# Kernel tuning notes

Hardware: AMD Instinct MI355X
Metric: run time of the kernel (lower is better)

## Reference

```python
import jax, jax.numpy as jnp
import numpy as np

B, S, D, H = 1, 4096, 1024, 16
HD = D // H  # head_dim = 64


def setup_inputs() -> dict:
    key = jax.random.key(0)
    k1, k2, k3 = jax.random.split(key, 3)
    scale = 0.02
    return {
        "x": jax.random.normal(k1, (B, S, D), dtype=jnp.float32),
        "w_qkv": jax.random.normal(k2, (D, 3 * D), dtype=jnp.float32) * scale,
        "b_qkv": jnp.zeros((3 * D,), dtype=jnp.float32),
        "w_proj": jax.random.normal(k3, (D, D), dtype=jnp.float32) * scale,
        "b_proj": jnp.zeros((D,), dtype=jnp.float32),
    }


def reference(x, w_qkv, b_qkv, w_proj, b_proj):
    b, s, d = x.shape
    qkv = x @ w_qkv + b_qkv                      # [b, s, 3d]
    q, k, v = jnp.split(qkv, 3, axis=-1)
    # [b, h, s, hd]
    q = q.reshape(b, s, H, HD).transpose(0, 2, 1, 3)
    k = k.reshape(b, s, H, HD).transpose(0, 2, 1, 3)
    v = v.reshape(b, s, H, HD).transpose(0, 2, 1, 3)
    score = jnp.einsum("bhqd,bhkd->bhqk", q, k) / jnp.sqrt(jnp.float32(HD))
    causal = jnp.tril(jnp.ones((s, s), dtype=bool))
    score = jnp.where(causal, score, -jnp.inf)
    attn = jax.nn.softmax(score, axis=-1)        # dropout omitted (eval mode, p effectively 0)
    out = jnp.einsum("bhqk,bhkd->bhqd", attn, v)  # [b, h, s, hd]
    out = out.transpose(0, 2, 1, 3).reshape(b, s, d)
    return out @ w_proj + b_proj
```

## Files before the change

kernel.cpp:

```cpp
#include <hip/hip_runtime.h>
#include <hip/hip_bf16.h>
#include <math.h>

typedef __bf16 bf16;
typedef __bf16 bf16x8 __attribute__((ext_vector_type(8)));
typedef __bf16 bf16x4 __attribute__((ext_vector_type(4)));
typedef float f32x4 __attribute__((ext_vector_type(4)));

#define S_ 4096
#define D_ 1024
#define H_ 16
#define HD_ 64
#define N3_ 3072

typedef const __attribute__((address_space(1))) void* gas1_t;
typedef __attribute__((address_space(3))) void* las3_t;
static __device__ __forceinline__ void g2l16(const void* g, void* l) {
  __builtin_amdgcn_global_load_lds((gas1_t)g, (las3_t)l, 16, 0, 0);
}

__global__ __launch_bounds__(256) void cvt_f32_bf16(const float* __restrict__ in,
                                                    bf16* __restrict__ out) {
  int i = (blockIdx.x * 256 + threadIdx.x) * 4;
  float4 v = *(const float4*)(in + i);
  bf16x4 o;
  o.x = (bf16)v.x; o.y = (bf16)v.y; o.z = (bf16)v.z; o.w = (bf16)v.w;
  *(bf16x4*)(out + i) = o;
}

__global__ __launch_bounds__(256) void transpose_f32_bf16(const float* __restrict__ in,
                                                          bf16* __restrict__ out,
                                                          int R, int C, int ldin, int col0) {
  __shared__ float t[32][33];
  int bx = blockIdx.x * 32;
  int by = blockIdx.y * 32;
  int tx = threadIdx.x & 31, ty = threadIdx.x >> 5;
#pragma unroll
  for (int i = 0; i < 4; ++i)
    t[ty + i * 8][tx] = in[(size_t)(by + ty + i * 8) * ldin + col0 + bx + tx];
  __syncthreads();
#pragma unroll
  for (int i = 0; i < 4; ++i)
    out[(size_t)(bx + ty + i * 8) * R + by + tx] = (bf16)t[tx][ty + i * 8];
}

__global__ __launch_bounds__(256) void transpose_bf16(const bf16* __restrict__ in,
                                                      bf16* __restrict__ out,
                                                      int R, int C, int ldin, int col0) {
  __shared__ bf16 t[32][33];
  int bx = blockIdx.x * 32;
  int by = blockIdx.y * 32;
  int tx = threadIdx.x & 31, ty = threadIdx.x >> 5;
#pragma unroll
  for (int i = 0; i < 4; ++i)
    t[ty + i * 8][tx] = in[(size_t)(by + ty + i * 8) * ldin + col0 + bx + tx];
  __syncthreads();
#pragma unroll
  for (int i = 0; i < 4; ++i)
    out[(size_t)(bx + ty + i * 8) * R + by + tx] = t[tx][ty + i * 8];
}

template <int BN>
__global__ __launch_bounds__(256) void gemm_bt(const bf16* __restrict__ A,
                                               const bf16* __restrict__ Bt,
                                               const float* __restrict__ bias,
                                               bf16* __restrict__ outb,
                                               float* __restrict__ outf,
                                               int M, int N, int K,
                                               int qlim, float qscale) {
  constexpr int NT = BN / 32;
  __shared__ bf16 sA[128 * 32];
  __shared__ bf16 sB[BN * 32];
  const int tid = threadIdx.x;
  const int wave = tid >> 6, lane = tid & 63;
  const int col = lane & 15, quad = lane >> 4;
  const int wm = (wave & 1) * 64, wn = (wave >> 1) * (BN / 2);
  const long bm = (long)blockIdx.x * 128, bn = (long)blockIdx.y * BN;
  const int srow = tid >> 2;
  const int soff = (tid & 3) * 8;

  f32x4 acc[4][NT] = {};

  for (int kb = 0; kb < K; kb += 32) {
    __syncthreads();
    g2l16(A + (bm + srow) * (long)K + kb + soff,      &sA[tid * 8]);
    g2l16(A + (bm + 64 + srow) * (long)K + kb + soff, &sA[2048 + tid * 8]);
#pragma unroll
    for (int i = 0; i < BN / 64; ++i)
      g2l16(Bt + (bn + i * 64 + srow) * (long)K + kb + soff, &sB[i * 2048 + tid * 8]);
    __syncthreads();

    bf16x8 af[4], bfr[NT];
#pragma unroll
    for (int t = 0; t < 4; ++t)
      af[t] = *(const bf16x8*)(&sA[(wm + t * 16 + col) * 32 + quad * 8]);
#pragma unroll
    for (int t = 0; t < NT; ++t)
      bfr[t] = *(const bf16x8*)(&sB[(wn + t * 16 + col) * 32 + quad * 8]);
#pragma unroll
    for (int mt = 0; mt < 4; ++mt)
#pragma unroll
      for (int nt = 0; nt < NT; ++nt)
        acc[mt][nt] = __builtin_amdgcn_mfma_f32_16x16x32_bf16(af[mt], bfr[nt], acc[mt][nt], 0, 0, 0);
  }

#pragma unroll
  for (int mt = 0; mt < 4; ++mt) {
#pragma unroll
    for (int nt = 0; nt < NT; ++nt) {
      long gn = bn + wn + nt * 16 + col;
      float bv = bias ? bias[gn] : 0.f;
      float sc = (gn < qlim) ? qscale : 1.0f;
#pragma unroll
      for (int i = 0; i < 4; ++i) {
        long gm = bm + wm + mt * 16 + quad * 4 + i;
        float v = (acc[mt][nt][i] + bv) * sc;
        if (outf) outf[gm * N + gn] = v;
        else      outb[gm * N + gn] = (bf16)v;
      }
    }
  }
}

__device__ __forceinline__ int swz_g(int row) {
  return (row & 3) | ((((row >> 2) ^ (row >> 3)) & 1) << 2);
}

__global__ __launch_bounds__(256) void attn_kernel(const bf16* __restrict__ qkv,
                                                   const bf16* __restrict__ vT,
                                                   bf16* __restrict__ Opart,
                                                   float* __restrict__ lws) {
  __shared__ bf16 sK[2][64 * 64];
  __shared__ bf16 sV[2][64 * 64];
  const int hh = blockIdx.x;
  const int qb = (int)(gridDim.y - 1 - blockIdx.y);
  const int sp = blockIdx.z;
  const int tid = threadIdx.x;
  const int wave = tid >> 6, lane = tid & 63;
  const int col = lane & 15, quad = lane >> 4;
  const int qbase = qb * 128 + wave * 32;

  const bf16* qp0 = qkv + (size_t)(qbase + col) * N3_ + hh * HD_;
  bf16x8 aq[2][2];
  aq[0][0] = *(const bf16x8*)(qp0 + quad * 8);
  aq[0][1] = *(const bf16x8*)(qp0 + 32 + quad * 8);
  aq[1][0] = *(const bf16x8*)(qp0 + 16 * N3_ + quad * 8);
  aq[1][1] = *(const bf16x8*)(qp0 + 16 * N3_ + 32 + quad * 8);

  bf16x8 ones;
#pragma unroll
  for (int j = 0; j < 8; ++j) ones[j] = (bf16)1.0f;

  f32x4 acc[2][4] = {};
  f32x4 acc_l[2] = {};

  const bf16* kgbase = qkv + D_ + hh * HD_;
  const bf16* vgbase = vT + (size_t)hh * HD_ * S_;
  const int krow = (col >> 2) * 8 + (col & 3);
  const int it0 = sp ? (qb + 1) : 0;
  const int it1 = sp ? 2 * (qb + 1) : (qb + 1);

  const int srow = tid >> 2;
  const int sc0 = (tid & 3) * 2;
  const int gs = swz_g(srow);
  const int soff0 = srow * 64 + ((sc0 ^ gs) * 8);
  const int soff1 = srow * 64 + (((sc0 + 1) ^ gs) * 8);

  {
    const bf16* kg = kgbase + (size_t)(it0 * 64 + srow) * N3_ + sc0 * 8;
    const bf16* vg = vgbase + (size_t)srow * S_ + it0 * 64 + sc0 * 8;
    *(int4*)(&sK[0][soff0]) = *(const int4*)kg;
    *(int4*)(&sK[0][soff1]) = *(const int4*)(kg + 8);
    *(int4*)(&sV[0][soff0]) = *(const int4*)vg;
    *(int4*)(&sV[0][soff1]) = *(const int4*)(vg + 8);
  }
  __syncthreads();

  for (int j = it0; j < it1; ++j) {
    const int kb = j * 64;
    const int cur = (j - it0) & 1;
    const bool more = (j + 1 < it1);
    int4 pk0, pk1, pv0, pv1;
    if (more) {
      const bf16* kg = kgbase + (size_t)(kb + 64 + srow) * N3_ + sc0 * 8;
      const bf16* vg = vgbase + (size_t)srow * S_ + kb + 64 + sc0 * 8;
      pk0 = *(const int4*)kg; pk1 = *(const int4*)(kg + 8);
      pv0 = *(const int4*)vg; pv1 = *(const int4*)(vg + 8);
    }

    if (kb < qbase + 32) {
      const bool act0 = kb < qbase + 16;
      const bf16* kc = &sK[cur][0];
      const bf16* vc = &sV[cur][0];

      f32x4 st[2][4];
#pragma unroll
      for (int t = 0; t < 4; ++t) {
        int row = (t >> 1) * 32 + (t & 1) * 4 + krow;
        int pc = quad ^ swz_g(row);
        bf16x8 bk0 = *(const bf16x8*)(kc + row * 64 + pc * 8);
        bf16x8 bk1 = *(const bf16x8*)(kc + row * 64 + (pc ^ 4) * 8);
        if (act0) {
          f32x4 z = {};
          z = __builtin_amdgcn_mfma_f32_16x16x32_bf16(bk0, aq[0][0], z, 0, 0, 0);
          st[0][t] = __builtin_amdgcn_mfma_f32_16x16x32_bf16(bk1, aq[0][1], z, 0, 0, 0);
        }
        f32x4 z = {};
        z = __builtin_amdgcn_mfma_f32_16x16x32_bf16(bk0, aq[1][0], z, 0, 0, 0);
        st[1][t] = __builtin_amdgcn_mfma_f32_16x16x32_bf16(bk1, aq[1][1], z, 0, 0, 0);
      }

      bf16x8 pfrag[2][2];
#pragma unroll
      for (int s2 = 0; s2 < 2; ++s2) {
        if (s2 == 0 && !act0) continue;
        const int rowbase = qbase + 16 * s2;
        float p[4][4];
        if (kb + 63 <= rowbase) {
#pragma unroll
          for (int t = 0; t < 4; ++t)
#pragma unroll
            for (int r = 0; r < 4; ++r)
              p[t][r] = __builtin_amdgcn_exp2f(st[s2][t][r]);
        } else {
#pragma unroll
          for (int t = 0; t < 4; ++t)
#pragma unroll
            for (int r = 0; r < 4; ++r) {
              int key = kb + (t >> 1) * 32 + quad * 8 + (t & 1) * 4 + r;
              p[t][r] = (key > rowbase + col)
                            ? 0.f
                            : __builtin_amdgcn_exp2f(st[s2][t][r]);
            }
        }
#pragma unroll
        for (int c = 0; c < 2; ++c)
#pragma unroll
          for (int j2 = 0; j2 < 4; ++j2) {
            pfrag[s2][c][j2]     = (bf16)p[2 * c][j2];
            pfrag[s2][c][j2 + 4] = (bf16)p[2 * c + 1][j2];
          }
      }

#pragma unroll
      for (int c = 0; c < 2; ++c) {
#pragma unroll
        for (int n = 0; n < 4; ++n) {
          int row = n * 16 + col;
          int pc = (4 * c + quad) ^ swz_g(row);
          bf16x8 bv = *(const bf16x8*)(vc + row * 64 + pc * 8);
          if (act0)
            acc[0][n] = __builtin_amdgcn_mfma_f32_16x16x32_bf16(pfrag[0][c], bv, acc[0][n], 0, 0, 0);
          acc[1][n] = __builtin_amdgcn_mfma_f32_16x16x32_bf16(pfrag[1][c], bv, acc[1][n], 0, 0, 0);
        }
        if (act0)
          acc_l[0] = __builtin_amdgcn_mfma_f32_16x16x32_bf16(pfrag[0][c], ones, acc_l[0], 0, 0, 0);
        acc_l[1] = __builtin_amdgcn_mfma_f32_16x16x32_bf16(pfrag[1][c], ones, acc_l[1], 0, 0, 0);
      }
    }

    if (more) {
      bf16* kn = &sK[cur ^ 1][0];
      bf16* vn = &sV[cur ^ 1][0];
      *(int4*)(kn + soff0) = pk0;
      *(int4*)(kn + soff1) = pk1;
      *(int4*)(vn + soff0) = pv0;
      *(int4*)(vn + soff1) = pv1;
    }
    __syncthreads();
  }

  bf16* Op = Opart + (size_t)sp * S_ * D_;
#pragma unroll
  for (int s2 = 0; s2 < 2; ++s2) {
    const int rowbase = qbase + 16 * s2;
    if (col == 0) {
#pragma unroll
      for (int r = 0; r < 4; ++r)
        lws[((size_t)sp * H_ + hh) * S_ + rowbase + quad * 4 + r] = acc_l[s2][r];
    }
#pragma unroll
    for (int n = 0; n < 4; ++n)
#pragma unroll
      for (int r = 0; r < 4; ++r)
        Op[(size_t)(rowbase + quad * 4 + r) * D_ + hh * HD_ + n * 16 + col] =
            (bf16)acc[s2][n][r];
  }
}

__global__ __launch_bounds__(256) void attn_combine(const bf16* __restrict__ Opart,
                                                    const float* __restrict__ lws,
                                                    bf16* __restrict__ outb) {
  int e = (blockIdx.x * 256 + threadIdx.x) * 8;
  int s = e >> 10;
  int d = e & (D_ - 1);
  int h = d >> 6;
  float l = lws[(size_t)h * S_ + s] + lws[((size_t)H_ + h) * S_ + s];
  float inv = 1.0f / l;
  bf16x8 a = *(const bf16x8*)(Opart + e);
  bf16x8 b = *(const bf16x8*)(Opart + (size_t)S_ * D_ + e);
  bf16x8 o;
#pragma unroll
  for (int j = 0; j < 8; ++j)
    o[j] = (bf16)(((float)a[j] + (float)b[j]) * inv);
  *(bf16x8*)(outb + e) = o;
}

extern "C" void kernel_launch(void* const* d_in, const int* in_sizes, int n_in,
                              void* d_out, int out_size, void* d_ws, size_t ws_size,
                              hipStream_t stream) {
  const float* x      = (const float*)d_in[0];
  const float* w_qkv  = (const float*)d_in[1];
  const float* b_qkv  = (const float*)d_in[2];
  const float* w_proj = (const float*)d_in[3];
  const float* b_proj = (const float*)d_in[4];
  float* out = (float*)d_out;

  bf16* xb     = (bf16*)d_ws;
  bf16* wqkvT  = xb + (size_t)S_ * D_;
  bf16* wprojT = wqkvT + (size_t)N3_ * D_;
  bf16* qkv    = wprojT + (size_t)D_ * D_;
  bf16* vT     = qkv + (size_t)S_ * N3_;
  bf16* attn   = vT + (size_t)D_ * S_;
  bf16* Opart  = attn + (size_t)S_ * D_;
  float* lws   = (float*)(Opart + (size_t)2 * S_ * D_);

  const float QSCALE = 0.125f * 1.44269504088896f;

  cvt_f32_bf16<<<dim3((S_ * D_) / 1024), 256, 0, stream>>>(x, xb);
  transpose_f32_bf16<<<dim3(N3_ / 32, D_ / 32), 256, 0, stream>>>(w_qkv, wqkvT, D_, N3_, N3_, 0);
  transpose_f32_bf16<<<dim3(D_ / 32, D_ / 32), 256, 0, stream>>>(w_proj, wprojT, D_, D_, D_, 0);
  gemm_bt<128><<<dim3(S_ / 128, N3_ / 128), 256, 0, stream>>>(
      xb, wqkvT, b_qkv, qkv, nullptr, S_, N3_, D_, D_, QSCALE);
  transpose_bf16<<<dim3(D_ / 32, S_ / 32), 256, 0, stream>>>(qkv, vT, S_, D_, N3_, 2 * D_);
  attn_kernel<<<dim3(H_, S_ / 128, 2), 256, 0, stream>>>(qkv, vT, Opart, lws);
  attn_combine<<<dim3((S_ * D_) / 2048), 256, 0, stream>>>(Opart, lws, attn);
  gemm_bt<64><<<dim3(S_ / 128, D_ / 64), 256, 0, stream>>>(
      attn, wprojT, b_proj, nullptr, out, S_, D_, D_, 0, 1.0f);
}
```

Measured before the change: 214.9 us.

## Split attention KV range four ways, fuse prep kernels, write V transposed from GEMM

Attention work per query block is now split into four balanced key-range chunks instead of two, so more blocks run and the causal load is spread more evenly. The combine kernel sums four partials to match. The three input conversion and transpose kernels are merged into one launch. The QKV GEMM epilogue writes the V columns directly in transposed layout, which removes the separate transpose pass. In exchange there are more partial outputs to write and read in the combine step, and the transposed V stores are strided.

```diff
diff --git a/kernel.cpp b/kernel.cpp
--- a/kernel.cpp
+++ b/kernel.cpp
@@ -12,6 +12,7 @@
 #define H_ 16
 #define HD_ 64
 #define N3_ 3072
+#define NSPLIT 4
 
 typedef const __attribute__((address_space(1))) void* gas1_t;
 typedef __attribute__((address_space(3))) void* las3_t;
@@ -19,45 +20,33 @@
   __builtin_amdgcn_global_load_lds((gas1_t)g, (las3_t)l, 16, 0, 0);
 }
 
-__global__ __launch_bounds__(256) void cvt_f32_bf16(const float* __restrict__ in,
-                                                    bf16* __restrict__ out) {
-  int i = (blockIdx.x * 256 + threadIdx.x) * 4;
-  float4 v = *(const float4*)(in + i);
-  bf16x4 o;
-  o.x = (bf16)v.x; o.y = (bf16)v.y; o.z = (bf16)v.z; o.w = (bf16)v.w;
-  *(bf16x4*)(out + i) = o;
-}
-
-__global__ __launch_bounds__(256) void transpose_f32_bf16(const float* __restrict__ in,
-                                                          bf16* __restrict__ out,
-                                                          int R, int C, int ldin, int col0) {
+__global__ __launch_bounds__(256) void prep_kernel(const float* __restrict__ x,
+                                                   bf16* __restrict__ xb,
+                                                   const float* __restrict__ w_qkv,
+                                                   bf16* __restrict__ wqkvT,
+                                                   const float* __restrict__ w_proj,
+                                                   bf16* __restrict__ wprojT) {
   __shared__ float t[32][33];
-  int bx = blockIdx.x * 32;
-  int by = blockIdx.y * 32;
-  int tx = threadIdx.x & 31, ty = threadIdx.x >> 5;
+  const int b = blockIdx.x;
+  if (b < 4096) {
+    int i = (b * 256 + threadIdx.x) * 4;
+    float4 v = *(const float4*)(x + i);
+    bf16x4 o;
+    o.x = (bf16)v.x; o.y = (bf16)v.y; o.z = (bf16)v.z; o.w = (bf16)v.w;
+    *(bf16x4*)(xb + i) = o;
+    return;
+  }
+  const float* in; bf16* outp; int ldin, bx, by;
+  if (b < 7168) { int b2 = b - 4096; in = w_qkv;  outp = wqkvT;  ldin = N3_; bx = (b2 % 96) * 32; by = (b2 / 96) * 32; }
+  else          { int b3 = b - 7168; in = w_proj; outp = wprojT; ldin = D_;  bx = (b3 % 32) * 32; by = (b3 / 32) * 32; }
+  const int tx = threadIdx.x & 31, ty = threadIdx.x >> 5;
 #pragma unroll
   for (int i = 0; i < 4; ++i)
-    t[ty + i * 8][tx] = in[(size_t)(by + ty + i * 8) * ldin + col0 + bx + tx];
+    t[ty + i * 8][tx] = in[(size_t)(by + ty + i * 8) * ldin + bx + tx];
   __syncthreads();
 #pragma unroll
   for (int i = 0; i < 4; ++i)
-    out[(size_t)(bx + ty + i * 8) * R + by + tx] = (bf16)t[tx][ty + i * 8];
-}
-
-__global__ __launch_bounds__(256) void transpose_bf16(const bf16* __restrict__ in,
-                                                      bf16* __restrict__ out,
-                                                      int R, int C, int ldin, int col0) {
-  __shared__ bf16 t[32][33];
-  int bx = blockIdx.x * 32;
-  int by = blockIdx.y * 32;
-  int tx = threadIdx.x & 31, ty = threadIdx.x >> 5;
-#pragma unroll
-  for (int i = 0; i < 4; ++i)
-    t[ty + i * 8][tx] = in[(size_t)(by + ty + i * 8) * ldin + col0 + bx + tx];
-  __syncthreads();
-#pragma unroll
-  for (int i = 0; i < 4; ++i)
-    out[(size_t)(bx + ty + i * 8) * R + by + tx] = t[tx][ty + i * 8];
+    outp[(size_t)(bx + ty + i * 8) * D_ + by + tx] = (bf16)t[tx][ty + i * 8];
 }
 
 template <int BN>
@@ -66,6 +55,7 @@
                                                const float* __restrict__ bias,
                                                bf16* __restrict__ outb,
                                                float* __restrict__ outf,
+                                               bf16* __restrict__ vTout,
                                                int M, int N, int K,
                                                int qlim, float qscale) {
   constexpr int NT = BN / 32;
@@ -110,13 +100,21 @@
     for (int nt = 0; nt < NT; ++nt) {
       long gn = bn + wn + nt * 16 + col;
       float bv = bias ? bias[gn] : 0.f;
-      float sc = (gn < qlim) ? qscale : 1.0f;
-#pragma unroll
-      for (int i = 0; i < 4; ++i) {
-        long gm = bm + wm + mt * 16 + quad * 4 + i;
-        float v = (acc[mt][nt][i] + bv) * sc;
-        if (outf) outf[gm * N + gn] = v;
-        else      outb[gm * N + gn] = (bf16)v;
+      if (vTout && gn >= 2 * D_) {
+        bf16x4 vv;
+        long gm0 = bm + wm + mt * 16 + quad * 4;
+#pragma unroll
+        for (int i = 0; i < 4; ++i) vv[i] = (bf16)(acc[mt][nt][i] + bv);
+        *(bf16x4*)(&vTout[(gn - 2 * D_) * (long)S_ + gm0]) = vv;
+      } else {
+        float sc = (gn < qlim) ? qscale : 1.0f;
+#pragma unroll
+        for (int i = 0; i < 4; ++i) {
+          long gm = bm + wm + mt * 16 + quad * 4 + i;
+          float v = (acc[mt][nt][i] + bv) * sc;
+          if (outf) outf[gm * N + gn] = v;
+          else      outb[gm * N + gn] = (bf16)v;
+        }
       }
     }
   }
@@ -157,8 +155,11 @@
   const bf16* kgbase = qkv + D_ + hh * HD_;
   const bf16* vgbase = vT + (size_t)hh * HD_ * S_;
   const int krow = (col >> 2) * 8 + (col & 3);
-  const int it0 = sp ? (qb + 1) : 0;
-  const int it1 = sp ? 2 * (qb + 1) : (qb + 1);
+  const int niter = 2 * (qb + 1);
+  const int base = niter >> 2, rem = niter & 3;
+  const int it0 = sp * base + (sp < rem ? sp : rem);
+  const int len = base + (sp < rem ? 1 : 0);
+  const int it1 = it0 + len;
 
   const int srow = tid >> 2;
   const int sc0 = (tid & 3) * 2;
@@ -166,108 +167,110 @@
   const int soff0 = srow * 64 + ((sc0 ^ gs) * 8);
   const int soff1 = srow * 64 + (((sc0 + 1) ^ gs) * 8);
 
-  {
-    const bf16* kg = kgbase + (size_t)(it0 * 64 + srow) * N3_ + sc0 * 8;
-    const bf16* vg = vgbase + (size_t)srow * S_ + it0 * 64 + sc0 * 8;
-    *(int4*)(&sK[0][soff0]) = *(const int4*)kg;
-    *(int4*)(&sK[0][soff1]) = *(const int4*)(kg + 8);
-    *(int4*)(&sV[0][soff0]) = *(const int4*)vg;
-    *(int4*)(&sV[0][soff1]) = *(const int4*)(vg + 8);
-  }
-  __syncthreads();
-
-  for (int j = it0; j < it1; ++j) {
-    const int kb = j * 64;
-    const int cur = (j - it0) & 1;
-    const bool more = (j + 1 < it1);
-    int4 pk0, pk1, pv0, pv1;
-    if (more) {
-      const bf16* kg = kgbase + (size_t)(kb + 64 + srow) * N3_ + sc0 * 8;
-      const bf16* vg = vgbase + (size_t)srow * S_ + kb + 64 + sc0 * 8;
-      pk0 = *(const int4*)kg; pk1 = *(const int4*)(kg + 8);
-      pv0 = *(const int4*)vg; pv1 = *(const int4*)(vg + 8);
+  if (len > 0) {
+    {
+      const bf16* kg = kgbase + (size_t)(it0 * 64 + srow) * N3_ + sc0 * 8;
+      const bf16* vg = vgbase + (size_t)srow * S_ + it0 * 64 + sc0 * 8;
+      *(int4*)(&sK[0][soff0]) = *(const int4*)kg;
+      *(int4*)(&sK[0][soff1]) = *(const int4*)(kg + 8);
+      *(int4*)(&sV[0][soff0]) = *(const int4*)vg;
+      *(int4*)(&sV[0][soff1]) = *(const int4*)(vg + 8);
     }
-
-    if (kb < qbase + 32) {
-      const bool act0 = kb < qbase + 16;
-      const bf16* kc = &sK[cur][0];
-      const bf16* vc = &sV[cur][0];
-
-      f32x4 st[2][4];
-#pragma unroll
-      for (int t = 0; t < 4; ++t) {
-        int row = (t >> 1) * 32 + (t & 1) * 4 + krow;
-        int pc = quad ^ swz_g(row);
-        bf16x8 bk0 = *(const bf16x8*)(kc + row * 64 + pc * 8);
-        bf16x8 bk1 = *(const bf16x8*)(kc + row * 64 + (pc ^ 4) * 8);
-        if (act0) {
+    __syncthreads();
+
+    for (int j = it0; j < it1; ++j) {
+      const int kb = j * 64;
+      const int cur = (j - it0) & 1;
+      const bool more = (j + 1 < it1);
+      int4 pk0, pk1, pv0, pv1;
+      if (more) {
+        const bf16* kg = kgbase + (size_t)(kb + 64 + srow) * N3_ + sc0 * 8;
+        const bf16* vg = vgbase + (size_t)srow * S_ + kb + 64 + sc0 * 8;
+        pk0 = *(const int4*)kg; pk1 = *(const int4*)(kg + 8);
+        pv0 = *(const int4*)vg; pv1 = *(const int4*)(vg + 8);
+      }
+
+      if (kb < qbase + 32) {
+        const bool act0 = kb < qbase + 16;
+        const bf16* kc = &sK[cur][0];
+        const bf16* vc = &sV[cur][0];
+
+        f32x4 st[2][4];
+#pragma unroll
+        for (int t = 0; t < 4; ++t) {
+          int row = (t >> 1) * 32 + (t & 1) * 4 + krow;
+          int pc = quad ^ swz_g(row);
+          bf16x8 bk0 = *(const bf16x8*)(kc + row * 64 + pc * 8);
+          bf16x8 bk1 = *(const bf16x8*)(kc + row * 64 + (pc ^ 4) * 8);
+          if (act0) {
+            f32x4 z = {};
+            z = __builtin_amdgcn_mfma_f32_16x16x32_bf16(bk0, aq[0][0], z, 0, 0, 0);
+            st[0][t] = __builtin_amdgcn_mfma_f32_16x16x32_bf16(bk1, aq[0][1], z, 0, 0, 0);
+          }
           f32x4 z = {};
-          z = __builtin_amdgcn_mfma_f32_16x16x32_bf16(bk0, aq[0][0], z, 0, 0, 0);
-          st[0][t] = __builtin_amdgcn_mfma_f32_16x16x32_bf16(bk1, aq[0][1], z, 0, 0, 0);
+          z = __builtin_amdgcn_mfma_f32_16x16x32_bf16(bk0, aq[1][0], z, 0, 0, 0);
+          st[1][t] = __builtin_amdgcn_mfma_f32_16x16x32_bf16(bk1, aq[1][1], z, 0, 0, 0);
         }
-        f32x4 z = {};
-        z = __builtin_amdgcn_mfma_f32_16x16x32_bf16(bk0, aq[1][0], z, 0, 0, 0);
-        st[1][t] = __builtin_amdgcn_mfma_f32_16x16x32_bf16(bk1, aq[1][1], z, 0, 0, 0);
-      }
-
-      bf16x8 pfrag[2][2];
-#pragma unroll
-      for (int s2 = 0; s2 < 2; ++s2) {
-        if (s2 == 0 && !act0) continue;
-        const int rowbase = qbase + 16 * s2;
-        float p[4][4];
-        if (kb + 63 <= rowbase) {
-#pragma unroll
-          for (int t = 0; t < 4; ++t)
-#pragma unroll
-            for (int r = 0; r < 4; ++r)
-              p[t][r] = __builtin_amdgcn_exp2f(st[s2][t][r]);
-        } else {
-#pragma unroll
-          for (int t = 0; t < 4; ++t)
-#pragma unroll
-            for (int r = 0; r < 4; ++r) {
-              int key = kb + (t >> 1) * 32 + quad * 8 + (t & 1) * 4 + r;
-              p[t][r] = (key > rowbase + col)
-                            ? 0.f
-                            : __builtin_amdgcn_exp2f(st[s2][t][r]);
+
+        bf16x8 pfrag[2][2];
+#pragma unroll
+        for (int s2 = 0; s2 < 2; ++s2) {
+          if (s2 == 0 && !act0) continue;
+          const int rowbase = qbase + 16 * s2;
+          float p[4][4];
+          if (kb + 63 <= rowbase) {
+#pragma unroll
+            for (int t = 0; t < 4; ++t)
+#pragma unroll
+              for (int r = 0; r < 4; ++r)
+                p[t][r] = __builtin_amdgcn_exp2f(st[s2][t][r]);
+          } else {
+#pragma unroll
+            for (int t = 0; t < 4; ++t)
+#pragma unroll
+              for (int r = 0; r < 4; ++r) {
+                int key = kb + (t >> 1) * 32 + quad * 8 + (t & 1) * 4 + r;
+                p[t][r] = (key > rowbase + col)
+                              ? 0.f
+                              : __builtin_amdgcn_exp2f(st[s2][t][r]);
+              }
+          }
+#pragma unroll
+          for (int c = 0; c < 2; ++c)
+#pragma unroll
+            for (int j2 = 0; j2 < 4; ++j2) {
+              pfrag[s2][c][j2]     = (bf16)p[2 * c][j2];
+              pfrag[s2][c][j2 + 4] = (bf16)p[2 * c + 1][j2];
             }
         }
-#pragma unroll
-        for (int c = 0; c < 2; ++c)
-#pragma unroll
-          for (int j2 = 0; j2 < 4; ++j2) {
-            pfrag[s2][c][j2]     = (bf16)p[2 * c][j2];
-            pfrag[s2][c][j2 + 4] = (bf16)p[2 * c + 1][j2];
+
+#pragma unroll
+        for (int c = 0; c < 2; ++c) {
+#pragma unroll
+          for (int n = 0; n < 4; ++n) {
+            int row = n * 16 + col;
+            int pc = (4 * c + quad) ^ swz_g(row);
+            bf16x8 bv = *(const bf16x8*)(vc + row * 64 + pc * 8);
+            if (act0)
+              acc[0][n] = __builtin_amdgcn_mfma_f32_16x16x32_bf16(pfrag[0][c], bv, acc[0][n], 0, 0, 0);
+            acc[1][n] = __builtin_amdgcn_mfma_f32_16x16x32_bf16(pfrag[1][c], bv, acc[1][n], 0, 0, 0);
           }
+          if (act0)
+            acc_l[0] = __builtin_amdgcn_mfma_f32_16x16x32_bf16(pfrag[0][c], ones, acc_l[0], 0, 0, 0);
+          acc_l[1] = __builtin_amdgcn_mfma_f32_16x16x32_bf16(pfrag[1][c], ones, acc_l[1], 0, 0, 0);
+        }
       }
 
-#pragma unroll
-      for (int c = 0; c < 2; ++c) {
-#pragma unroll
-        for (int n = 0; n < 4; ++n) {
-          int row = n * 16 + col;
-          int pc = (4 * c + quad) ^ swz_g(row);
-          bf16x8 bv = *(const bf16x8*)(vc + row * 64 + pc * 8);
-          if (act0)
-            acc[0][n] = __builtin_amdgcn_mfma_f32_16x16x32_bf16(pfrag[0][c], bv, acc[0][n], 0, 0, 0);
-          acc[1][n] = __builtin_amdgcn_mfma_f32_16x16x32_bf16(pfrag[1][c], bv, acc[1][n], 0, 0, 0);
-        }
-        if (act0)
-          acc_l[0] = __builtin_amdgcn_mfma_f32_16x16x32_bf16(pfrag[0][c], ones, acc_l[0], 0, 0, 0);
-        acc_l[1] = __builtin_amdgcn_mfma_f32_16x16x32_bf16(pfrag[1][c], ones, acc_l[1], 0, 0, 0);
+      if (more) {
+        bf16* kn = &sK[cur ^ 1][0];
+        bf16* vn = &sV[cur ^ 1][0];
+        *(int4*)(kn + soff0) = pk0;
+        *(int4*)(kn + soff1) = pk1;
+        *(int4*)(vn + soff0) = pv0;
+        *(int4*)(vn + soff1) = pv1;
       }
+      __syncthreads();
     }
-
-    if (more) {
-      bf16* kn = &sK[cur ^ 1][0];
-      bf16* vn = &sV[cur ^ 1][0];
-      *(int4*)(kn + soff0) = pk0;
-      *(int4*)(kn + soff1) = pk1;
-      *(int4*)(vn + soff0) = pv0;
-      *(int4*)(vn + soff1) = pv1;
-    }
-    __syncthreads();
   }
 
   bf16* Op = Opart + (size_t)sp * S_ * D_;
@@ -293,17 +296,22 @@
                                                     bf16* __restrict__ outb) {
   int e = (blockIdx.x * 256 + threadIdx.x) * 8;
   int s = e >> 10;
-  int d = e & (D_ - 1);
-  int h = d >> 6;
-  float l = lws[(size_t)h * S_ + s] + lws[((size_t)H_ + h) * S_ + s];
+  int h = (e & (D_ - 1)) >> 6;
+  float l = 0.f;
+#pragma unroll
+  for (int sp = 0; sp < NSPLIT; ++sp) l += lws[((size_t)sp * H_ + h) * S_ + s];
   float inv = 1.0f / l;
-  bf16x8 a = *(const bf16x8*)(Opart + e);
-  bf16x8 b = *(const bf16x8*)(Opart + (size_t)S_ * D_ + e);
-  bf16x8 o;
-#pragma unroll
-  for (int j = 0; j < 8; ++j)
-    o[j] = (bf16)(((float)a[j] + (float)b[j]) * inv);
-  *(bf16x8*)(outb + e) = o;
+  float o[8] = {};
+#pragma unroll
+  for (int sp = 0; sp < NSPLIT; ++sp) {
+    bf16x8 a = *(const bf16x8*)(Opart + (size_t)sp * S_ * D_ + e);
+#pragma unroll
+    for (int j = 0; j < 8; ++j) o[j] += (float)a[j];
+  }
+  bf16x8 r;
+#pragma unroll
+  for (int j = 0; j < 8; ++j) r[j] = (bf16)(o[j] * inv);
+  *(bf16x8*)(outb + e) = r;
 }
 
 extern "C" void kernel_launch(void* const* d_in, const int* in_sizes, int n_in,
@@ -321,20 +329,17 @@
   bf16* wprojT = wqkvT + (size_t)N3_ * D_;
   bf16* qkv    = wprojT + (size_t)D_ * D_;
   bf16* vT     = qkv + (size_t)S_ * N3_;
-  bf16* attn   = vT + (size_t)D_ * S_;
-  bf16* Opart  = attn + (size_t)S_ * D_;
-  float* lws   = (float*)(Opart + (size_t)2 * S_ * D_);
+  bf16* Opart  = vT + (size_t)D_ * S_;
+  float* lws   = (float*)(Opart + (size_t)NSPLIT * S_ * D_);
+  bf16* attn   = xb;
 
   const float QSCALE = 0.125f * 1.44269504088896f;
 
-  cvt_f32_bf16<<<dim3((S_ * D_) / 1024), 256, 0, stream>>>(x, xb);
-  transpose_f32_bf16<<<dim3(N3_ / 32, D_ / 32), 256, 0, stream>>>(w_qkv, wqkvT, D_, N3_, N3_, 0);
-  transpose_f32_bf16<<<dim3(D_ / 32, D_ / 32), 256, 0, stream>>>(w_proj, wprojT, D_, D_, D_, 0);
+  prep_kernel<<<dim3(8192), 256, 0, stream>>>(x, xb, w_qkv, wqkvT, w_proj, wprojT);
   gemm_bt<128><<<dim3(S_ / 128, N3_ / 128), 256, 0, stream>>>(
-      xb, wqkvT, b_qkv, qkv, nullptr, S_, N3_, D_, D_, QSCALE);
-  transpose_bf16<<<dim3(D_ / 32, S_ / 32), 256, 0, stream>>>(qkv, vT, S_, D_, N3_, 2 * D_);
-  attn_kernel<<<dim3(H_, S_ / 128, 2), 256, 0, stream>>>(qkv, vT, Opart, lws);
+      xb, wqkvT, b_qkv, qkv, nullptr, vT, S_, N3_, D_, D_, QSCALE);
+  attn_kernel<<<dim3(H_, S_ / 128, NSPLIT), 256, 0, stream>>>(qkv, vT, Opart, lws);
   attn_combine<<<dim3((S_ * D_) / 2048), 256, 0, stream>>>(Opart, lws, attn);
   gemm_bt<64><<<dim3(S_ / 128, D_ / 64), 256, 0, stream>>>(
-      attn, wprojT, b_proj, nullptr, out, S_, D_, D_, 0, 1.0f);
-}
+      attn, wprojT, b_proj, nullptr, out, nullptr, S_, D_, D_, 0, 1.0f);
+}
```

Result: no change. 212.3 us (-1.2%).
